# Optimization experiments

Measured on AMD Instinct MI355X. Metric: run time of the kernel, lower is better.

Reference implementation:

```python
import jax, jax.numpy as jnp
import numpy as np

N_NODES = 16384
D_IN = 256
D_OUT = 256
AVG_DEG = 32


def setup_inputs() -> dict:
    key = jax.random.key(0)
    kx, ka, kw, kb = jax.random.split(key, 4)
    x = jax.random.normal(kx, (N_NODES, D_IN), dtype=jnp.float32)
    # Binary dense adjacency with average degree ~AVG_DEG (matches `adj[i] > 0` usage).
    adj = (jax.random.uniform(ka, (N_NODES, N_NODES)) < (AVG_DEG / N_NODES)).astype(jnp.float32)
    # nn.Linear(2*in_features, out_features): weight [out, 2*in], bias [out]
    W = jax.random.normal(kw, (D_OUT, 2 * D_IN), dtype=jnp.float32) * (1.0 / np.sqrt(2 * D_IN))
    b = jnp.zeros((D_OUT,), dtype=jnp.float32)
    return {"x": x, "adj": adj, "W": W, "b": b, "sample_size": 10}


def reference(x, adj, W, b, sample_size):
    # Vectorized equivalent of the per-node loop:
    # sample min(deg, sample_size) neighbors uniformly without replacement,
    # mean-aggregate, concat with self features, linear + relu.
    key = jax.random.key(42)
    noise = jax.random.uniform(key, adj.shape)            # [N, N]
    # Gumbel-top-k trick: top-k uniform scores over neighbors == uniform sample w/o replacement.
    scores = jnp.where(adj > 0, noise, -jnp.inf)
    top_scores, top_idx = jax.lax.top_k(scores, sample_size)  # [N, k]
    valid = jnp.isfinite(top_scores)                          # [N, k] false where deg < k
    feats = x[top_idx] * valid[..., None].astype(x.dtype)     # [N, k, d]
    cnt = valid.sum(axis=-1, keepdims=True).astype(x.dtype)   # [N, 1]
    agg = feats.sum(axis=1) / jnp.maximum(cnt, 1.0)           # mean; zeros if no neighbors
    h = jnp.concatenate([x, agg], axis=-1)                    # [N, 2d]
    return jax.nn.relu(h @ W.T + b)
```

## Files before the change

### kernel.cpp

```cpp
#include <hip/hip_runtime.h>
#include <hip/hip_bf16.h>
#include <stdint.h>

#define N_NODES 16384
#define D_IN    256
#define D_OUT   256
#define K_SAMP  10
#define HALF_FLAT (1u << 27)

#define JAX_PARTITIONABLE 1

typedef __attribute__((ext_vector_type(4))) float  f32x4;
typedef __attribute__((ext_vector_type(8))) short  bf16x8;
typedef __attribute__((ext_vector_type(4))) int    i32x4;

__device__ __forceinline__ uint32_t rotl32(uint32_t x, int r) {
    return (x << r) | (x >> (32 - r));
}

__device__ __forceinline__ uint32_t jax_noise_bits(uint32_t r, uint32_t c) {
    const uint32_t i  = (r << 14) | c;
    const uint32_t k0 = 0u, k1 = 42u;
    const uint32_t k2 = 42u ^ 0x1BD11BDAu;
    uint32_t x0, x1;
#if JAX_PARTITIONABLE
    x0 = 0u;
    x1 = i;
#else
    const bool lo = (i < HALF_FLAT);
    x0 = lo ? i : (i - HALF_FLAT);
    x1 = lo ? (i + HALF_FLAT) : i;
#endif
    x0 += k0; x1 += k1;
#define TFR4(a,b,cc,d) \
    x0 += x1; x1 = rotl32(x1,a);  x1 ^= x0; \
    x0 += x1; x1 = rotl32(x1,b);  x1 ^= x0; \
    x0 += x1; x1 = rotl32(x1,cc); x1 ^= x0; \
    x0 += x1; x1 = rotl32(x1,d);  x1 ^= x0;
    TFR4(13,15,26,6);   x0 += k1; x1 += k2 + 1u;
    TFR4(17,29,16,24);  x0 += k2; x1 += k0 + 2u;
    TFR4(13,15,26,6);   x0 += k0; x1 += k1 + 3u;
    TFR4(17,29,16,24);  x0 += k1; x1 += k2 + 4u;
    TFR4(13,15,26,6);   x0 += k2; x1 += k0 + 5u;
#undef TFR4
#if JAX_PARTITIONABLE
    return x0 ^ x1;
#else
    return (i < HALF_FLAT) ? x0 : x1;
#endif
}

__device__ __forceinline__ unsigned short f2bfbits(float f) {
    __hip_bfloat16 h = __float2bfloat16(f);
    return *(unsigned short*)&h;
}

__global__ __launch_bounds__(256) void k_agg(
    const float* __restrict__ x, const float* __restrict__ adj,
    unsigned short* __restrict__ h)
{
    const int t    = threadIdx.x;
    const int lane = t & 63;
    const int w    = t >> 6;
    const int r    = blockIdx.x * 4 + w;

    __shared__ unsigned short candc[4][128];

    const f32x4* rowp = (const f32x4*)(adj + (size_t)r * N_NODES);
    int nc = 0;
    #pragma unroll 8
    for (int it = 0; it < 64; ++it) {
        f32x4 v = __builtin_nontemporal_load(rowp + it * 64 + lane);
        int cb = (it * 64 + lane) * 4;
        #pragma unroll
        for (int j = 0; j < 4; ++j) {
            unsigned long long mask = __ballot(v[j] != 0.0f);
            if (mask) {
                if (v[j] != 0.0f) {
                    int below = __builtin_amdgcn_mbcnt_hi(
                        (uint32_t)(mask >> 32),
                        __builtin_amdgcn_mbcnt_lo((uint32_t)mask, 0));
                    int slot = nc + below;
                    if (slot < 128) candc[w][slot] = (unsigned short)(cb + j);
                }
                nc += __popcll(mask);
            }
        }
    }
    __syncthreads();
    if (nc > 128) nc = 128;

    unsigned long long k0 = 0ull, k1 = 0ull;
    if (lane < nc) {
        uint32_t c   = candc[w][lane];
        uint32_t u23 = jax_noise_bits((uint32_t)r, c) >> 9;
        k0 = ((((unsigned long long)u23) << 14) | (unsigned long long)(16383u - c)) + 1ull;
    }
    if (64 + lane < nc) {
        uint32_t c   = candc[w][64 + lane];
        uint32_t u23 = jax_noise_bits((uint32_t)r, c) >> 9;
        k1 = ((((unsigned long long)u23) << 14) | (unsigned long long)(16383u - c)) + 1ull;
    }

    const int m = nc < K_SAMP ? nc : K_SAMP;
    f32x4 acc = {0.f, 0.f, 0.f, 0.f};
    for (int s = 0; s < m; ++s) {
        unsigned long long my = k0 > k1 ? k0 : k1;
        #pragma unroll
        for (int o = 1; o < 64; o <<= 1) {
            unsigned long long other = __shfl_xor(my, o);
            if (other > my) my = other;
        }
        if (k0 == my) k0 = 0ull; else if (k1 == my) k1 = 0ull;
        const int col = 16383 - (int)((my - 1ull) & 0x3FFFull);
        f32x4 xv = *(const f32x4*)(x + (size_t)col * D_IN + lane * 4);
        acc += xv;
    }
    const float inv = (m > 0) ? 1.0f / (float)m : 0.0f;

    f32x4 sv = *(const f32x4*)(x + (size_t)r * D_IN + lane * 4);
    ushort4 us, ua;
    us.x = f2bfbits(sv[0]);        us.y = f2bfbits(sv[1]);
    us.z = f2bfbits(sv[2]);        us.w = f2bfbits(sv[3]);
    ua.x = f2bfbits(acc[0] * inv); ua.y = f2bfbits(acc[1] * inv);
    ua.z = f2bfbits(acc[2] * inv); ua.w = f2bfbits(acc[3] * inv);
    unsigned short* hr = h + (size_t)r * (2 * D_IN);
    *(ushort4*)(hr + lane * 4)         = us;
    *(ushort4*)(hr + D_IN + lane * 4)  = ua;
}

__global__ __launch_bounds__(256) void k_convw(const float* __restrict__ W,
                                               unsigned short* __restrict__ Wb)
{
    int i = (blockIdx.x * 256 + threadIdx.x) * 4;
    float4 v = *(const float4*)(W + i);
    ushort4 u;
    u.x = f2bfbits(v.x); u.y = f2bfbits(v.y); u.z = f2bfbits(v.z); u.w = f2bfbits(v.w);
    *(ushort4*)(Wb + i) = u;
}

#define BM 64
#define BN 64
#define BK 64

__global__ __launch_bounds__(256) void k_gemm(
    const unsigned short* __restrict__ h, const unsigned short* __restrict__ Wb,
    const float* __restrict__ bias, float* __restrict__ out)
{
    __shared__ short As[2][BM * BK];
    __shared__ short Bs[2][BN * BK];

    const int t    = threadIdx.x;
    const int lane = t & 63;
    const int wv   = t >> 6;
    const int wr   = wv >> 1;
    const int wc   = wv & 1;
    const int m0   = blockIdx.x * BM;
    const int n0   = blockIdx.y * BN;
    const int lr   = lane & 15;
    const int lk   = lane >> 4;

    f32x4 acc[2][2] = {};

    const short* hA = (const short*)h;
    const short* wB = (const short*)Wb;

    const int q0  = t, q1 = t + 256;
    const int r0  = q0 >> 3, c0 = q0 & 7;
    const int r1  = q1 >> 3, c1 = q1 & 7;
    const int ba0 = (r0 * 128 + c0 * 16) ^ ((r0 & 7) << 4);
    const int ba1 = (r1 * 128 + c1 * 16) ^ ((r1 & 7) << 4);

    {
        i32x4 a0 = *(const i32x4*)(hA + (size_t)(m0 + r0) * 512 + c0 * 8);
        i32x4 a1 = *(const i32x4*)(hA + (size_t)(m0 + r1) * 512 + c1 * 8);
        i32x4 b0 = *(const i32x4*)(wB + (size_t)(n0 + r0) * 512 + c0 * 8);
        i32x4 b1 = *(const i32x4*)(wB + (size_t)(n0 + r1) * 512 + c1 * 8);
        *(i32x4*)((char*)&As[0][0] + ba0) = a0;
        *(i32x4*)((char*)&As[0][0] + ba1) = a1;
        *(i32x4*)((char*)&Bs[0][0] + ba0) = b0;
        *(i32x4*)((char*)&Bs[0][0] + ba1) = b1;
    }
    __syncthreads();

    for (int tt = 0; tt < 8; ++tt) {
        const int cur = tt & 1;
        i32x4 a0, a1, b0, b1;
        if (tt < 7) {
            const int k0n = (tt + 1) * BK;
            a0 = *(const i32x4*)(hA + (size_t)(m0 + r0) * 512 + k0n + c0 * 8);
            a1 = *(const i32x4*)(hA + (size_t)(m0 + r1) * 512 + k0n + c1 * 8);
            b0 = *(const i32x4*)(wB + (size_t)(n0 + r0) * 512 + k0n + c0 * 8);
            b1 = *(const i32x4*)(wB + (size_t)(n0 + r1) * 512 + k0n + c1 * 8);
        }

        #pragma unroll
        for (int kk = 0; kk < BK; kk += 32) {
            bf16x8 af[2], bf[2];
            #pragma unroll
            for (int mi = 0; mi < 2; ++mi) {
                int row = wr * 32 + mi * 16 + lr;
                int ba = (row * 128 + (kk + lk * 8) * 2) ^ ((row & 7) << 4);
                af[mi] = *(const bf16x8*)((const char*)&As[cur][0] + ba);
            }
            #pragma unroll
            for (int ni = 0; ni < 2; ++ni) {
                int row = wc * 32 + ni * 16 + lr;
                int ba = (row * 128 + (kk + lk * 8) * 2) ^ ((row & 7) << 4);
                bf[ni] = *(const bf16x8*)((const char*)&Bs[cur][0] + ba);
            }
            #pragma unroll
            for (int mi = 0; mi < 2; ++mi)
                #pragma unroll
                for (int ni = 0; ni < 2; ++ni)
                    acc[mi][ni] = __builtin_amdgcn_mfma_f32_16x16x32_bf16(
                        af[mi], bf[ni], acc[mi][ni], 0, 0, 0);
        }

        if (tt < 7) {
            const int nxt = cur ^ 1;
            *(i32x4*)((char*)&As[nxt][0] + ba0) = a0;
            *(i32x4*)((char*)&As[nxt][0] + ba1) = a1;
            *(i32x4*)((char*)&Bs[nxt][0] + ba0) = b0;
            *(i32x4*)((char*)&Bs[nxt][0] + ba1) = b1;
        }
        __syncthreads();
    }

    #pragma unroll
    for (int mi = 0; mi < 2; ++mi) {
        #pragma unroll
        for (int ni = 0; ni < 2; ++ni) {
            int col = n0 + wc * 32 + ni * 16 + lr;
            float bv = bias[col];
            #pragma unroll
            for (int j = 0; j < 4; ++j) {
                int rowg = m0 + wr * 32 + mi * 16 + lk * 4 + j;
                float v = acc[mi][ni][j] + bv;
                out[(size_t)rowg * D_OUT + col] = v > 0.0f ? v : 0.0f;
            }
        }
    }
}

extern "C" void kernel_launch(void* const* d_in, const int* in_sizes, int n_in,
                              void* d_out, int out_size, void* d_ws, size_t ws_size,
                              hipStream_t stream) {
    (void)in_sizes; (void)n_in; (void)out_size; (void)ws_size;
    const float* x   = (const float*)d_in[0];
    const float* adj = (const float*)d_in[1];
    const float* W   = (const float*)d_in[2];
    const float* b   = (const float*)d_in[3];

    unsigned short* hbuf = (unsigned short*)d_ws;
    unsigned short* Wb   = (unsigned short*)((char*)d_ws + (size_t)N_NODES * 512 * 2);
    float* out = (float*)d_out;

    hipLaunchKernelGGL(k_convw, dim3((D_OUT * 2 * D_IN) / 1024), dim3(256), 0, stream, W, Wb);
    hipLaunchKernelGGL(k_agg,   dim3(N_NODES / 4), dim3(256), 0, stream, x, adj, hbuf);
    hipLaunchKernelGGL(k_gemm,  dim3(N_NODES / BM, D_OUT / BN), dim3(256), 0, stream,
                       hbuf, Wb, b, out);
}
```

Before: 220.0 us.

## Fuse aggregation with per-row linear layer, drop MFMA GEMM and h buffer

Replaces the separate bf16 MFMA GEMM with a per-wave FMA matvec inside the aggregation kernel. Each wave keeps its row's concatenated features in LDS and multiplies them against a transposed bf16 weight copy. This removes the round trip of the h intermediate through global memory and one kernel launch. In exchange, every row rereads the full 256 KB weight matrix from cache and uses scalar FMAs instead of matrix cores. It also drops a __syncthreads, which is safe only because LDS use stays within each wave.

```diff
diff --git a/kernel.cpp b/kernel.cpp
--- a/kernel.cpp
+++ b/kernel.cpp
@@ -11,8 +11,6 @@
 #define JAX_PARTITIONABLE 1
 
 typedef __attribute__((ext_vector_type(4))) float  f32x4;
-typedef __attribute__((ext_vector_type(8))) short  bf16x8;
-typedef __attribute__((ext_vector_type(4))) int    i32x4;
 
 __device__ __forceinline__ uint32_t rotl32(uint32_t x, int r) {
     return (x << r) | (x >> (32 - r));
@@ -55,9 +53,32 @@
     return *(unsigned short*)&h;
 }
 
-__global__ __launch_bounds__(256) void k_agg(
+__global__ __launch_bounds__(256) void k_transw(const float* __restrict__ W,
+                                                unsigned short* __restrict__ Wt)
+{
+    __shared__ float tile[32][33];
+    const int tx = threadIdx.x;
+    const int ty = threadIdx.y;
+    const int kb = blockIdx.x * 32;
+    const int nb = blockIdx.y * 32;
+
+    #pragma unroll
+    for (int i = 0; i < 4; ++i) {
+        int n = ty + 8 * i;
+        tile[n][tx] = W[(size_t)(nb + n) * 512 + kb + tx];
+    }
+    __syncthreads();
+    #pragma unroll
+    for (int i = 0; i < 4; ++i) {
+        int k = ty + 8 * i;
+        Wt[(size_t)(kb + k) * 256 + nb + tx] = f2bfbits(tile[tx][k]);
+    }
+}
+
+__global__ __launch_bounds__(256) void k_fused(
     const float* __restrict__ x, const float* __restrict__ adj,
-    unsigned short* __restrict__ h)
+    const unsigned short* __restrict__ Wt, const float* __restrict__ bias,
+    float* __restrict__ out)
 {
     const int t    = threadIdx.x;
     const int lane = t & 63;
@@ -65,6 +86,7 @@
     const int r    = blockIdx.x * 4 + w;
 
     __shared__ unsigned short candc[4][128];
+    __shared__ float hL[4][512];
 
     const f32x4* rowp = (const f32x4*)(adj + (size_t)r * N_NODES);
     int nc = 0;
@@ -87,7 +109,6 @@
             }
         }
     }
-    __syncthreads();
     if (nc > 128) nc = 128;
 
     unsigned long long k0 = 0ull, k1 = 0ull;
@@ -119,128 +140,31 @@
     const float inv = (m > 0) ? 1.0f / (float)m : 0.0f;
 
     f32x4 sv = *(const f32x4*)(x + (size_t)r * D_IN + lane * 4);
-    ushort4 us, ua;
-    us.x = f2bfbits(sv[0]);        us.y = f2bfbits(sv[1]);
-    us.z = f2bfbits(sv[2]);        us.w = f2bfbits(sv[3]);
-    ua.x = f2bfbits(acc[0] * inv); ua.y = f2bfbits(acc[1] * inv);
-    ua.z = f2bfbits(acc[2] * inv); ua.w = f2bfbits(acc[3] * inv);
-    unsigned short* hr = h + (size_t)r * (2 * D_IN);
-    *(ushort4*)(hr + lane * 4)         = us;
-    *(ushort4*)(hr + D_IN + lane * 4)  = ua;
-}
+    *(f32x4*)&hL[w][lane * 4]         = sv;
+    f32x4 av = acc * inv;
+    *(f32x4*)&hL[w][D_IN + lane * 4]  = av;
 
-__global__ __launch_bounds__(256) void k_convw(const float* __restrict__ W,
-                                               unsigned short* __restrict__ Wb)
-{
-    int i = (blockIdx.x * 256 + threadIdx.x) * 4;
-    float4 v = *(const float4*)(W + i);
-    ushort4 u;
-    u.x = f2bfbits(v.x); u.y = f2bfbits(v.y); u.z = f2bfbits(v.z); u.w = f2bfbits(v.w);
-    *(ushort4*)(Wb + i) = u;
-}
-
-#define BM 64
-#define BN 64
-#define BK 64
-
-__global__ __launch_bounds__(256) void k_gemm(
-    const unsigned short* __restrict__ h, const unsigned short* __restrict__ Wb,
-    const float* __restrict__ bias, float* __restrict__ out)
-{
-    __shared__ short As[2][BM * BK];
-    __shared__ short Bs[2][BN * BK];
-
-    const int t    = threadIdx.x;
-    const int lane = t & 63;
-    const int wv   = t >> 6;
-    const int wr   = wv >> 1;
-    const int wc   = wv & 1;
-    const int m0   = blockIdx.x * BM;
-    const int n0   = blockIdx.y * BN;
-    const int lr   = lane & 15;
-    const int lk   = lane >> 4;
-
-    f32x4 acc[2][2] = {};
-
-    const short* hA = (const short*)h;
-    const short* wB = (const short*)Wb;
-
-    const int q0  = t, q1 = t + 256;
-    const int r0  = q0 >> 3, c0 = q0 & 7;
-    const int r1  = q1 >> 3, c1 = q1 & 7;
-    const int ba0 = (r0 * 128 + c0 * 16) ^ ((r0 & 7) << 4);
-    const int ba1 = (r1 * 128 + c1 * 16) ^ ((r1 & 7) << 4);
-
-    {
-        i32x4 a0 = *(const i32x4*)(hA + (size_t)(m0 + r0) * 512 + c0 * 8);
-        i32x4 a1 = *(const i32x4*)(hA + (size_t)(m0 + r1) * 512 + c1 * 8);
-        i32x4 b0 = *(const i32x4*)(wB + (size_t)(n0 + r0) * 512 + c0 * 8);
-        i32x4 b1 = *(const i32x4*)(wB + (size_t)(n0 + r1) * 512 + c1 * 8);
-        *(i32x4*)((char*)&As[0][0] + ba0) = a0;
-        *(i32x4*)((char*)&As[0][0] + ba1) = a1;
-        *(i32x4*)((char*)&Bs[0][0] + ba0) = b0;
-        *(i32x4*)((char*)&Bs[0][0] + ba1) = b1;
-    }
-    __syncthreads();
-
-    for (int tt = 0; tt < 8; ++tt) {
-        const int cur = tt & 1;
-        i32x4 a0, a1, b0, b1;
-        if (tt < 7) {
-            const int k0n = (tt + 1) * BK;
-            a0 = *(const i32x4*)(hA + (size_t)(m0 + r0) * 512 + k0n + c0 * 8);
-            a1 = *(const i32x4*)(hA + (size_t)(m0 + r1) * 512 + k0n + c1 * 8);
-            b0 = *(const i32x4*)(wB + (size_t)(n0 + r0) * 512 + k0n + c0 * 8);
-            b1 = *(const i32x4*)(wB + (size_t)(n0 + r1) * 512 + k0n + c1 * 8);
-        }
-
+    const unsigned short* wp = Wt + lane * 4;
+    f32x4 o = {0.f, 0.f, 0.f, 0.f};
+    #pragma unroll 4
+    for (int kc = 0; kc < 128; ++kc) {
+        f32x4 hv = *(const f32x4*)&hL[w][kc * 4];
         #pragma unroll
-        for (int kk = 0; kk < BK; kk += 32) {
-            bf16x8 af[2], bf[2];
-            #pragma unroll
-            for (int mi = 0; mi < 2; ++mi) {
-                int row = wr * 32 + mi * 16 + lr;
-                int ba = (row * 128 + (kk + lk * 8) * 2) ^ ((row & 7) << 4);
-                af[mi] = *(const bf16x8*)((const char*)&As[cur][0] + ba);
-            }
-            #pragma unroll
-            for (int ni = 0; ni < 2; ++ni) {
-                int row = wc * 32 + ni * 16 + lr;
-                int ba = (row * 128 + (kk + lk * 8) * 2) ^ ((row & 7) << 4);
-                bf[ni] = *(const bf16x8*)((const char*)&Bs[cur][0] + ba);
-            }
-            #pragma unroll
-            for (int mi = 0; mi < 2; ++mi)
-                #pragma unroll
-                for (int ni = 0; ni < 2; ++ni)
-                    acc[mi][ni] = __builtin_amdgcn_mfma_f32_16x16x32_bf16(
-                        af[mi], bf[ni], acc[mi][ni], 0, 0, 0);
-        }
-
-        if (tt < 7) {
-            const int nxt = cur ^ 1;
-            *(i32x4*)((char*)&As[nxt][0] + ba0) = a0;
-            *(i32x4*)((char*)&As[nxt][0] + ba1) = a1;
-            *(i32x4*)((char*)&Bs[nxt][0] + ba0) = b0;
-            *(i32x4*)((char*)&Bs[nxt][0] + ba1) = b1;
-        }
-        __syncthreads();
-    }
-
-    #pragma unroll
-    for (int mi = 0; mi < 2; ++mi) {
-        #pragma unroll
-        for (int ni = 0; ni < 2; ++ni) {
-            int col = n0 + wc * 32 + ni * 16 + lr;
-            float bv = bias[col];
-            #pragma unroll
-            for (int j = 0; j < 4; ++j) {
-                int rowg = m0 + wr * 32 + mi * 16 + lk * 4 + j;
-                float v = acc[mi][ni][j] + bv;
-                out[(size_t)rowg * D_OUT + col] = v > 0.0f ? v : 0.0f;
-            }
+        for (int j = 0; j < 4; ++j) {
+            uint2 wu = *(const uint2*)(wp + (size_t)(kc * 4 + j) * 256);
+            f32x4 wf;
+            wf[0] = __uint_as_float(wu.x << 16);
+            wf[1] = __uint_as_float(wu.x & 0xFFFF0000u);
+            wf[2] = __uint_as_float(wu.y << 16);
+            wf[3] = __uint_as_float(wu.y & 0xFFFF0000u);
+            o += hv[j] * wf;
         }
     }
+    f32x4 bv = *(const f32x4*)(bias + lane * 4);
+    o += bv;
+    #pragma unroll
+    for (int j = 0; j < 4; ++j) o[j] = o[j] > 0.f ? o[j] : 0.f;
+    __builtin_nontemporal_store(o, (f32x4*)(out + (size_t)r * D_OUT + lane * 4));
 }
 
 extern "C" void kernel_launch(void* const* d_in, const int* in_sizes, int n_in,
@@ -252,12 +176,10 @@
     const float* W   = (const float*)d_in[2];
     const float* b   = (const float*)d_in[3];
 
-    unsigned short* hbuf = (unsigned short*)d_ws;
-    unsigned short* Wb   = (unsigned short*)((char*)d_ws + (size_t)N_NODES * 512 * 2);
+    unsigned short* Wt = (unsigned short*)d_ws;
     float* out = (float*)d_out;
 
-    hipLaunchKernelGGL(k_convw, dim3((D_OUT * 2 * D_IN) / 1024), dim3(256), 0, stream, W, Wb);
-    hipLaunchKernelGGL(k_agg,   dim3(N_NODES / 4), dim3(256), 0, stream, x, adj, hbuf);
-    hipLaunchKernelGGL(k_gemm,  dim3(N_NODES / BM, D_OUT / BN), dim3(256), 0, stream,
-                       hbuf, Wb, b, out);
+    hipLaunchKernelGGL(k_transw, dim3(512 / 32, 256 / 32), dim3(32, 8), 0, stream, W, Wt);
+    hipLaunchKernelGGL(k_fused,  dim3(N_NODES / 4), dim3(256), 0, stream,
+                       x, adj, Wt, b, out);
 }
```

Result: slower. 400.9 us (+82.2%).
